# Performance work log

Hardware: AMD Instinct MI355X
Metric: run time of the kernel (lower is better)

The kernel has to match this reference:

```python
import jax, jax.numpy as jnp
import numpy as np

B, L, INP, HID = 32, 1024, 600, 200

def setup_inputs() -> dict:
    key = jax.random.key(0)
    k1, k2, k3, k4 = jax.random.split(key, 4)
    return {
        "s1": jax.random.normal(k1, (B, L, INP), dtype=jnp.float32),
        "s2": jax.random.normal(k2, (B, L, INP), dtype=jnp.float32),
        "mask1": jnp.ones((B, L), dtype=jnp.float32),
        "mask2": jnp.ones((B, L), dtype=jnp.float32),
        "W1": jax.random.normal(k3, (INP, HID), dtype=jnp.float32) * (1.0 / np.sqrt(INP)),
        "b1": jnp.zeros((HID,), dtype=jnp.float32),
        "W2": jax.random.normal(k4, (HID, HID), dtype=jnp.float32) * (1.0 / np.sqrt(HID)),
        "b2": jnp.zeros((HID,), dtype=jnp.float32),
    }

def _mlp(x, W1, b1, W2, b2):
    # Dropout is identity at inference; two Linear+ReLU layers.
    h = jax.nn.relu(x @ W1 + b1)
    return jax.nn.relu(h @ W2 + b2)

def reference(s1, s2, mask1, mask2, W1, b1, W2, b2):
    h1 = _mlp(s1, W1, b1, W2, b2)          # (b, L, hid)
    h2 = _mlp(s2, W1, b1, W2, b2)          # (b, L, hid)
    e = jnp.einsum('bld,bmd->blm', h1, h2) # (b, LA, LB)
    # alpha: mask rows by mask1, softmax over LA (axis=1)
    e_alpha = jax.nn.softmax(e * mask1[:, :, None], axis=1)
    # beta: mask cols by mask2, softmax over LB (axis=2)
    e_beta = jax.nn.softmax(e * mask2[:, None, :], axis=2)
    alphas = jnp.einsum('blm,bld->bmd', e_alpha, s1) * mask2[:, :, None]
    betas = jnp.einsum('blm,bmd->bld', e_beta, s2) * mask1[:, :, None]
    return alphas, betas
```

## Files before the change

kernel.cpp:

```cpp
#include <hip/hip_runtime.h>
#include <hip/hip_bf16.h>
#include <math.h>

namespace {

constexpr int BB  = 32;
constexpr int LL  = 1024;
constexpr int INP = 600;
constexpr int HID = 200;
constexpr int RS  = BB * LL;
constexpr int DPAD = 640;

constexpr int BM = 128, BN = 128, KT = 8;
constexpr int LROW = 40;

typedef __attribute__((ext_vector_type(8))) short short8v;
typedef __attribute__((ext_vector_type(4))) float f32x4;

__device__ __forceinline__ float relu(float x) { return fmaxf(x, 0.f); }

__device__ __forceinline__ unsigned short f2bf(float x) {
  union { float f; unsigned int u; } v; v.f = x;
  unsigned int r = v.u + 0x7FFFu + ((v.u >> 16) & 1u);
  return (unsigned short)(r >> 16);
}
__device__ __forceinline__ float bf2f(unsigned short h) {
  union { unsigned int u; float f; } v; v.u = ((unsigned int)h) << 16;
  return v.f;
}

__device__ __forceinline__ void micro_8x8(const float (&sA)[KT][BM], const float (&sB)[KT][BN],
                                          float (&acc)[8][8], int tx, int ty)
{
#pragma unroll
  for (int kk = 0; kk < KT; ++kk) {
    float4 a0 = *(const float4*)&sA[kk][ty * 8];
    float4 a1 = *(const float4*)&sA[kk][ty * 8 + 4];
    float4 b0 = *(const float4*)&sB[kk][tx * 8];
    float4 b1 = *(const float4*)&sB[kk][tx * 8 + 4];
    float ar[8] = {a0.x, a0.y, a0.z, a0.w, a1.x, a1.y, a1.z, a1.w};
    float br[8] = {b0.x, b0.y, b0.z, b0.w, b1.x, b1.y, b1.z, b1.w};
#pragma unroll
    for (int i = 0; i < 8; ++i)
#pragma unroll
      for (int j = 0; j < 8; ++j)
        acc[i][j] = fmaf(ar[i], br[j], acc[i][j]);
  }
}

__global__ __launch_bounds__(256) void wt_prep(
    const float* __restrict__ W, unsigned short* __restrict__ Whi, unsigned short* __restrict__ Wlo,
    int K, int KP)
{
  const int k = blockIdx.x * 256 + threadIdx.x;
  const int n = blockIdx.y;
  if (k >= KP) return;
  float v = (k < K && n < HID) ? W[(size_t)k * HID + n] : 0.f;
  unsigned short hi = f2bf(v);
  unsigned short lo = f2bf(v - bf2f(hi));
  Whi[(size_t)n * KP + k] = hi;
  Wlo[(size_t)n * KP + k] = lo;
}

__global__ __launch_bounds__(256) void mlp1_gemm_split(
    const float* __restrict__ A0, const float* __restrict__ A1,
    const unsigned short* __restrict__ Bhi, const unsigned short* __restrict__ Blo,
    const float* __restrict__ bias,
    unsigned short* __restrict__ OutHi, unsigned short* __restrict__ OutLo)
{
  __shared__ unsigned short sAhi[128 * LROW], sAlo[128 * LROW];
  __shared__ unsigned short sBhi[128 * LROW], sBlo[128 * LROW];
  const int z = blockIdx.z;
  const float* __restrict__ A = z ? A1 : A0;
  unsigned short* __restrict__ oH = OutHi + (size_t)z * RS * HID;
  unsigned short* __restrict__ oL = OutLo + (size_t)z * RS * HID;
  const int m0 = blockIdx.x * 128, n0 = blockIdx.y * 128;
  const int tid = threadIdx.x, lane = tid & 63;
  const int w = tid >> 6, wr = w >> 1, wc = w & 1;
  const int fr = lane & 15, kg = lane >> 4;

  f32x4 acc[4][4];
#pragma unroll
  for (int mi = 0; mi < 4; ++mi)
#pragma unroll
    for (int ni = 0; ni < 4; ++ni) acc[mi][ni] = (f32x4){0.f, 0.f, 0.f, 0.f};

  for (int k0 = 0; k0 < 608; k0 += 32) {
    __syncthreads();
#pragma unroll
    for (int it = 0; it < 4; ++it) {
      {
        const int t = it * 256 + tid;
        const int r = t >> 3, hc = t & 7;
        const int gk = k0 + hc * 4;
        float4 v = make_float4(0.f, 0.f, 0.f, 0.f);
        if (gk < INP) v = *(const float4*)(A + (size_t)(m0 + r) * INP + gk);
        ushort4 hi, lo;
        hi.x = f2bf(v.x); lo.x = f2bf(v.x - bf2f(hi.x));
        hi.y = f2bf(v.y); lo.y = f2bf(v.y - bf2f(hi.y));
        hi.z = f2bf(v.z); lo.z = f2bf(v.z - bf2f(hi.z));
        hi.w = f2bf(v.w); lo.w = f2bf(v.w - bf2f(hi.w));
        *(ushort4*)&sAhi[r * LROW + hc * 4] = hi;
        *(ushort4*)&sAlo[r * LROW + hc * 4] = lo;
      }
      {
        const int t = it * 256 + tid;
        const bool isLo = t >> 9;
        const int rem = t & 511, r = rem >> 2, c = rem & 3;
        const unsigned short* src = isLo ? Blo : Bhi;
        unsigned short* dst = isLo ? sBlo : sBhi;
        *(int4*)&dst[r * LROW + c * 8] = *(const int4*)(src + (size_t)(n0 + r) * 608 + k0 + c * 8);
      }
    }
    __syncthreads();
    short8v ah[4], al[4], bh[4], bl[4];
#pragma unroll
    for (int mi = 0; mi < 4; ++mi) {
      const int row = wr * 64 + mi * 16 + fr;
      ah[mi] = *(const short8v*)&sAhi[row * LROW + kg * 8];
      al[mi] = *(const short8v*)&sAlo[row * LROW + kg * 8];
    }
#pragma unroll
    for (int ni = 0; ni < 4; ++ni) {
      const int row = wc * 64 + ni * 16 + fr;
      bh[ni] = *(const short8v*)&sBhi[row * LROW + kg * 8];
      bl[ni] = *(const short8v*)&sBlo[row * LROW + kg * 8];
    }
#pragma unroll
    for (int mi = 0; mi < 4; ++mi)
#pragma unroll
      for (int ni = 0; ni < 4; ++ni) {
        acc[mi][ni] = __builtin_amdgcn_mfma_f32_16x16x32_bf16(ah[mi], bh[ni], acc[mi][ni], 0, 0, 0);
        acc[mi][ni] = __builtin_amdgcn_mfma_f32_16x16x32_bf16(ah[mi], bl[ni], acc[mi][ni], 0, 0, 0);
        acc[mi][ni] = __builtin_amdgcn_mfma_f32_16x16x32_bf16(al[mi], bh[ni], acc[mi][ni], 0, 0, 0);
      }
  }
#pragma unroll
  for (int ni = 0; ni < 4; ++ni) {
    const int gn = n0 + wc * 64 + ni * 16 + fr;
    if (gn < HID) {
      const float bs = bias[gn];
#pragma unroll
      for (int mi = 0; mi < 4; ++mi) {
#pragma unroll
        for (int r = 0; r < 4; ++r) {
          const int gm = m0 + wr * 64 + mi * 16 + kg * 4 + r;
          float v = relu(acc[mi][ni][r] + bs);
          unsigned short hi = f2bf(v);
          oH[(size_t)gm * HID + gn] = hi;
          oL[(size_t)gm * HID + gn] = f2bf(v - bf2f(hi));
        }
      }
    }
  }
}

template <bool SPLIT_OUT>
__global__ __launch_bounds__(256) void split_gemm_bf16(
    const unsigned short* __restrict__ Ahi, const unsigned short* __restrict__ Alo,
    int lda, size_t aZ,
    const unsigned short* __restrict__ Bhi, const unsigned short* __restrict__ Blo,
    int ldb, size_t bZ,
    int a_chunks, int b_chunks,
    const float* __restrict__ bias,
    unsigned short* __restrict__ OutHi, unsigned short* __restrict__ OutLo,
    float* __restrict__ OutF, int ldo, size_t oZ)
{
  __shared__ unsigned short sAhi[128 * LROW], sAlo[128 * LROW];
  __shared__ unsigned short sBhi[128 * LROW], sBlo[128 * LROW];
  const int z = blockIdx.z;
  const unsigned short* __restrict__ Ah = Ahi + (size_t)z * aZ;
  const unsigned short* __restrict__ Al = Alo + (size_t)z * aZ;
  const unsigned short* __restrict__ Bh = Bhi + (size_t)z * bZ;
  const unsigned short* __restrict__ Bl = Blo + (size_t)z * bZ;
  const int m0 = blockIdx.x * 128, n0 = blockIdx.y * 128;
  const int tid = threadIdx.x, lane = tid & 63;
  const int w = tid >> 6, wr = w >> 1, wc = w & 1;
  const int fr = lane & 15, kg = lane >> 4;

  f32x4 acc[4][4];
#pragma unroll
  for (int mi = 0; mi < 4; ++mi)
#pragma unroll
    for (int ni = 0; ni < 4; ++ni) acc[mi][ni] = (f32x4){0.f, 0.f, 0.f, 0.f};

  for (int k0 = 0; k0 < 224; k0 += 32) {
    const int kc0 = k0 >> 3;
    __syncthreads();
#pragma unroll
    for (int it = 0; it < 4; ++it) {
      const int t = it * 256 + tid;
      const bool isLo = t >> 9;
      const int rem = t & 511, r = rem >> 2, c = rem & 3;
      const bool av = (kc0 + c) < a_chunks;
      const bool bv = (kc0 + c) < b_chunks;
      int4 va = make_int4(0, 0, 0, 0), vb = make_int4(0, 0, 0, 0);
      if (av) va = *(const int4*)((isLo ? Al : Ah) + (size_t)(m0 + r) * lda + k0 + c * 8);
      if (bv) vb = *(const int4*)((isLo ? Bl : Bh) + (size_t)(n0 + r) * ldb + k0 + c * 8);
      unsigned short* dA = isLo ? sAlo : sAhi;
      unsigned short* dB = isLo ? sBlo : sBhi;
      *(int4*)&dA[r * LROW + c * 8] = va;
      *(int4*)&dB[r * LROW + c * 8] = vb;
    }
    __syncthreads();
    short8v ah[4], al[4], bh[4], bl[4];
#pragma unroll
    for (int mi = 0; mi < 4; ++mi) {
      const int row = wr * 64 + mi * 16 + fr;
      ah[mi] = *(const short8v*)&sAhi[row * LROW + kg * 8];
      al[mi] = *(const short8v*)&sAlo[row * LROW + kg * 8];
    }
#pragma unroll
    for (int ni = 0; ni < 4; ++ni) {
      const int row = wc * 64 + ni * 16 + fr;
      bh[ni] = *(const short8v*)&sBhi[row * LROW + kg * 8];
      bl[ni] = *(const short8v*)&sBlo[row * LROW + kg * 8];
    }
#pragma unroll
    for (int mi = 0; mi < 4; ++mi)
#pragma unroll
      for (int ni = 0; ni < 4; ++ni) {
        acc[mi][ni] = __builtin_amdgcn_mfma_f32_16x16x32_bf16(ah[mi], bh[ni], acc[mi][ni], 0, 0, 0);
        acc[mi][ni] = __builtin_amdgcn_mfma_f32_16x16x32_bf16(ah[mi], bl[ni], acc[mi][ni], 0, 0, 0);
        acc[mi][ni] = __builtin_amdgcn_mfma_f32_16x16x32_bf16(al[mi], bh[ni], acc[mi][ni], 0, 0, 0);
      }
  }
#pragma unroll
  for (int ni = 0; ni < 4; ++ni) {
    const int gn = n0 + wc * 64 + ni * 16 + fr;
    if (!SPLIT_OUT || gn < HID) {
      const float bs = SPLIT_OUT ? bias[gn] : 0.f;
#pragma unroll
      for (int mi = 0; mi < 4; ++mi) {
#pragma unroll
        for (int r = 0; r < 4; ++r) {
          const int gm = m0 + wr * 64 + mi * 16 + kg * 4 + r;
          if (SPLIT_OUT) {
            float v = relu(acc[mi][ni][r] + bs);
            unsigned short hi = f2bf(v);
            OutHi[(size_t)z * oZ + (size_t)gm * ldo + gn] = hi;
            OutLo[(size_t)z * oZ + (size_t)gm * ldo + gn] = f2bf(v - bf2f(hi));
          } else {
            OutF[(size_t)z * oZ + (size_t)gm * ldo + gn] = acc[mi][ni][r];
          }
        }
      }
    }
  }
}

__global__ __launch_bounds__(256) void row_stats_pbeta(
    const float* __restrict__ E, const float* __restrict__ mask2,
    unsigned short* __restrict__ Pb)
{
  const int wid = threadIdx.x >> 6, lane = threadIdx.x & 63;
  const int r = blockIdx.x * 4 + wid;
  const int b = r >> 10;
  const float* __restrict__ row = E + (size_t)r * LL;
  const float* __restrict__ m2 = mask2 + b * LL;
  float v[16];
  float mx = -INFINITY;
#pragma unroll
  for (int i = 0; i < 4; ++i) {
    const int m = lane * 4 + i * 256;
    float4 e4 = *(const float4*)(row + m);
    float4 k4 = *(const float4*)(m2 + m);
    v[i * 4 + 0] = e4.x * k4.x; v[i * 4 + 1] = e4.y * k4.y;
    v[i * 4 + 2] = e4.z * k4.z; v[i * 4 + 3] = e4.w * k4.w;
    mx = fmaxf(mx, fmaxf(fmaxf(v[i * 4], v[i * 4 + 1]), fmaxf(v[i * 4 + 2], v[i * 4 + 3])));
  }
#pragma unroll
  for (int off = 32; off; off >>= 1) mx = fmaxf(mx, __shfl_xor(mx, off));
  float s = 0.f;
#pragma unroll
  for (int i = 0; i < 16; ++i) s += __expf(v[i] - mx);
#pragma unroll
  for (int off = 32; off; off >>= 1) s += __shfl_xor(s, off);
  const float ri = 1.f / s;
#pragma unroll
  for (int i = 0; i < 4; ++i) {
    const int m = lane * 4 + i * 256;
    ushort4 o;
    o.x = f2bf(__expf(v[i * 4 + 0] - mx) * ri);
    o.y = f2bf(__expf(v[i * 4 + 1] - mx) * ri);
    o.z = f2bf(__expf(v[i * 4 + 2] - mx) * ri);
    o.w = f2bf(__expf(v[i * 4 + 3] - mx) * ri);
    *(ushort4*)(Pb + (size_t)r * LL + m) = o;
  }
}

__global__ __launch_bounds__(256) void col_stats_p1(
    const float* __restrict__ E, const float* __restrict__ mask1,
    float* __restrict__ pmax, float* __restrict__ psum)
{
  const int b = blockIdx.z, lc = blockIdx.y;
  const int m = blockIdx.x * 256 + threadIdx.x;
  const float* __restrict__ e = E + (size_t)b * LL * LL;
  const float* __restrict__ m1 = mask1 + b * LL;
  float mx = -INFINITY, s = 0.f;
#pragma unroll 4
  for (int l = lc * 256; l < lc * 256 + 256; ++l) {
    const float v = e[(size_t)l * LL + m] * m1[l];
    if (v > mx) { s = s * __expf(mx - v) + 1.f; mx = v; }
    else        { s += __expf(v - mx); }
  }
  const int idx = (b * 4 + lc) * LL + m;
  pmax[idx] = mx; psum[idx] = s;
}

__global__ __launch_bounds__(256) void col_stats_p2(
    const float* __restrict__ pmax, const float* __restrict__ psum,
    float* __restrict__ cmax, float* __restrict__ cinv)
{
  const int b = blockIdx.y;
  const int m = blockIdx.x * 256 + threadIdx.x;
  float M = -INFINITY;
#pragma unroll
  for (int i = 0; i < 4; ++i) M = fmaxf(M, pmax[(b * 4 + i) * LL + m]);
  float S = 0.f;
#pragma unroll
  for (int i = 0; i < 4; ++i) S += psum[(b * 4 + i) * LL + m] * __expf(pmax[(b * 4 + i) * LL + m] - M);
  cmax[(size_t)b * LL + m] = M;
  cinv[(size_t)b * LL + m] = 1.f / S;
}

__global__ __launch_bounds__(256) void palpha_kernel(
    const float* __restrict__ E, const float* __restrict__ mask1,
    const float* __restrict__ cmax, const float* __restrict__ cinv,
    unsigned short* __restrict__ Pa)
{
  __shared__ float T[64][65];
  const int b = blockIdx.z;
  const int l0 = blockIdx.y * 64, m0 = blockIdx.x * 64;
  const int tid = threadIdx.x;
  const int rr = tid >> 4, c4 = (tid & 15) * 4;
  const float4 cm = *(const float4*)(cmax + b * LL + m0 + c4);
  const float4 ci = *(const float4*)(cinv + b * LL + m0 + c4);
#pragma unroll
  for (int it = 0; it < 4; ++it) {
    const int lloc = rr + it * 16;
    const int l = l0 + lloc;
    const float mk = mask1[b * LL + l];
    const float4 ev = *(const float4*)(E + ((size_t)b * LL + l) * LL + m0 + c4);
    T[c4 + 0][lloc] = __expf(ev.x * mk - cm.x) * ci.x;
    T[c4 + 1][lloc] = __expf(ev.y * mk - cm.y) * ci.y;
    T[c4 + 2][lloc] = __expf(ev.z * mk - cm.z) * ci.z;
    T[c4 + 3][lloc] = __expf(ev.w * mk - cm.w) * ci.w;
  }
  __syncthreads();
#pragma unroll
  for (int it = 0; it < 4; ++it) {
    const int mloc = rr + it * 16;
    ushort4 o;
    o.x = f2bf(T[mloc][c4 + 0]);
    o.y = f2bf(T[mloc][c4 + 1]);
    o.z = f2bf(T[mloc][c4 + 2]);
    o.w = f2bf(T[mloc][c4 + 3]);
    *(ushort4*)(Pa + ((size_t)b * LL + m0 + mloc) * LL + l0 + c4) = o;
  }
}

__global__ __launch_bounds__(256) void s_transpose(
    const float* __restrict__ S, unsigned short* __restrict__ St)
{
  __shared__ float T[64][65];
  const int b = blockIdx.z;
  const int l0 = blockIdx.y * 64, d0 = blockIdx.x * 64;
  const int tid = threadIdx.x;
  const int rr = tid >> 4, c4 = (tid & 15) * 4;
#pragma unroll
  for (int it = 0; it < 4; ++it) {
    const int lloc = rr + it * 16;
    const int l = l0 + lloc;
    float4 v = make_float4(0.f, 0.f, 0.f, 0.f);
    if (d0 + c4 < INP) v = *(const float4*)(S + ((size_t)b * LL + l) * INP + d0 + c4);
    T[c4 + 0][lloc] = v.x; T[c4 + 1][lloc] = v.y;
    T[c4 + 2][lloc] = v.z; T[c4 + 3][lloc] = v.w;
  }
  __syncthreads();
#pragma unroll
  for (int it = 0; it < 4; ++it) {
    const int dloc = rr + it * 16;
    ushort4 o;
    o.x = f2bf(T[dloc][c4 + 0]);
    o.y = f2bf(T[dloc][c4 + 1]);
    o.z = f2bf(T[dloc][c4 + 2]);
    o.w = f2bf(T[dloc][c4 + 3]);
    *(ushort4*)(St + ((size_t)b * DPAD + d0 + dloc) * LL + l0 + c4) = o;
  }
}

__global__ __launch_bounds__(256) void attn_gemm_bf16(
    const unsigned short* __restrict__ Ap, const unsigned short* __restrict__ Bt,
    const float* __restrict__ scale, float* __restrict__ Out)
{
  __shared__ int4 sA4[1024];
  __shared__ int4 sB4[1024];
  __shared__ float s_sc[128];
  const int b  = blockIdx.z;
  const int n0 = blockIdx.x * 128;
  const int m0 = blockIdx.y * 128;
  const int tid = threadIdx.x;
  const int lane = tid & 63;
  const int w = tid >> 6;
  const int wr = w >> 1, wc = w & 1;

  const unsigned short* __restrict__ A  = Ap + (size_t)b * LL * LL;
  const unsigned short* __restrict__ Bp = Bt + (size_t)b * DPAD * LL;

  if (tid < 128) s_sc[tid] = scale[b * LL + m0 + tid];

  f32x4 acc[4][4];
#pragma unroll
  for (int mi = 0; mi < 4; ++mi)
#pragma unroll
    for (int ni = 0; ni < 4; ++ni)
      acc[mi][ni] = (f32x4){0.f, 0.f, 0.f, 0.f};

  const int kc = tid & 7;
  const int rbase = tid >> 3;
  const int fr = lane & 15;
  const int kg = lane >> 4;

  for (int k0 = 0; k0 < LL; k0 += 64) {
    __syncthreads();
#pragma unroll
    for (int it = 0; it < 4; ++it) {
      const int r = rbase + 32 * it;
      sA4[r * 8 + (kc ^ (r & 7))] = *(const int4*)(A  + (size_t)(m0 + r) * LL + k0 + kc * 8);
      sB4[r * 8 + (kc ^ (r & 7))] = *(const int4*)(Bp + (size_t)(n0 + r) * LL + k0 + kc * 8);
    }
    __syncthreads();
#pragma unroll
    for (int kk = 0; kk < 2; ++kk) {
      short8v a[4], bf[4];
#pragma unroll
      for (int mi = 0; mi < 4; ++mi) {
        const int row = wr * 64 + mi * 16 + fr;
        a[mi] = *(const short8v*)&sA4[row * 8 + ((kk * 4 + kg) ^ (row & 7))];
      }
#pragma unroll
      for (int ni = 0; ni < 4; ++ni) {
        const int row = wc * 64 + ni * 16 + fr;
        bf[ni] = *(const short8v*)&sB4[row * 8 + ((kk * 4 + kg) ^ (row & 7))];
      }
#pragma unroll
      for (int mi = 0; mi < 4; ++mi)
#pragma unroll
        for (int ni = 0; ni < 4; ++ni)
          acc[mi][ni] = __builtin_amdgcn_mfma_f32_16x16x32_bf16(a[mi], bf[ni], acc[mi][ni], 0, 0, 0);
    }
  }

#pragma unroll
  for (int mi = 0; mi < 4; ++mi) {
#pragma unroll
    for (int ni = 0; ni < 4; ++ni) {
      const int col = n0 + wc * 64 + ni * 16 + fr;
      if (col < INP) {
#pragma unroll
        for (int r = 0; r < 4; ++r) {
          const int mrow = wr * 64 + mi * 16 + kg * 4 + r;
          Out[((size_t)b * LL + m0 + mrow) * INP + col] = acc[mi][ni][r] * s_sc[mrow];
        }
      }
    }
  }
}

__global__ __launch_bounds__(256) void mlp_gemm(
    const float* __restrict__ A0, const float* __restrict__ A1,
    const float* __restrict__ W,  const float* __restrict__ bias,
    float* __restrict__ Out, int K)
{
  __shared__ __align__(16) float sA[KT][BM];
  __shared__ __align__(16) float sB[KT][BN];
  const int z = blockIdx.z;
  const float* __restrict__ A = z ? A1 : A0;
  float* __restrict__ out = Out + (size_t)z * RS * HID;
  const int m0 = blockIdx.x * BM;
  const int n0 = blockIdx.y * BN;
  const int tid = threadIdx.x;
  const int tx = tid & 15, ty = tid >> 4;
  const int am = tid & 127, akg = (tid >> 7) * 4;
  const int bn = (tid & 31) * 4, bkk = tid >> 5;

  float acc[8][8] = {};
  for (int k0 = 0; k0 < K; k0 += KT) {
    float4 av = *(const float4*)(A + (size_t)(m0 + am) * K + k0 + akg);
    sA[akg + 0][am] = av.x; sA[akg + 1][am] = av.y;
    sA[akg + 2][am] = av.z; sA[akg + 3][am] = av.w;
    const int gn = n0 + bn;
    float4 bv = make_float4(0.f, 0.f, 0.f, 0.f);
    if (gn < HID) bv = *(const float4*)(W + (size_t)(k0 + bkk) * HID + gn);
    *(float4*)&sB[bkk][bn] = bv;
    __syncthreads();
    micro_8x8(sA, sB, acc, tx, ty);
    __syncthreads();
  }
#pragma unroll
  for (int i = 0; i < 8; ++i) {
    const int m = m0 + ty * 8 + i;
#pragma unroll
    for (int j4 = 0; j4 < 8; j4 += 4) {
      const int n = n0 + tx * 8 + j4;
      if (n < HID) {
        float4 v;
        v.x = relu(acc[i][j4 + 0] + bias[n + 0]);
        v.y = relu(acc[i][j4 + 1] + bias[n + 1]);
        v.z = relu(acc[i][j4 + 2] + bias[n + 2]);
        v.w = relu(acc[i][j4 + 3] + bias[n + 3]);
        *(float4*)(out + (size_t)m * HID + n) = v;
      }
    }
  }
}

__global__ __launch_bounds__(256) void e_gemm(
    const float* __restrict__ H1, const float* __restrict__ H2, float* __restrict__ E)
{
  __shared__ __align__(16) float sA[KT][BM];
  __shared__ __align__(16) float sB[KT][BN];
  const int b = blockIdx.z;
  const float* __restrict__ A  = H1 + (size_t)b * LL * HID;
  const float* __restrict__ Bp = H2 + (size_t)b * LL * HID;
  float* __restrict__ e = E + (size_t)b * LL * LL;
  const int l0 = blockIdx.x * BM;
  const int m0 = blockIdx.y * BN;
  const int tid = threadIdx.x;
  const int tx = tid & 15, ty = tid >> 4;
  const int rr = tid & 127, kg = (tid >> 7) * 4;

  float acc[8][8] = {};
  for (int k0 = 0; k0 < HID; k0 += KT) {
    float4 av = *(const float4*)(A + (size_t)(l0 + rr) * HID + k0 + kg);
    sA[kg + 0][rr] = av.x; sA[kg + 1][rr] = av.y;
    sA[kg + 2][rr] = av.z; sA[kg + 3][rr] = av.w;
    float4 bv = *(const float4*)(Bp + (size_t)(m0 + rr) * HID + k0 + kg);
    sB[kg + 0][rr] = bv.x; sB[kg + 1][rr] = bv.y;
    sB[kg + 2][rr] = bv.z; sB[kg + 3][rr] = bv.w;
    __syncthreads();
    micro_8x8(sA, sB, acc, tx, ty);
    __syncthreads();
  }
#pragma unroll
  for (int i = 0; i < 8; ++i) {
    float* erow = e + (size_t)(l0 + ty * 8 + i) * LL + m0 + tx * 8;
    *(float4*)(erow)     = make_float4(acc[i][0], acc[i][1], acc[i][2], acc[i][3]);
    *(float4*)(erow + 4) = make_float4(acc[i][4], acc[i][5], acc[i][6], acc[i][7]);
  }
}

__global__ __launch_bounds__(256) void row_stats(
    const float* __restrict__ E, const float* __restrict__ mask2,
    float* __restrict__ rmax, float* __restrict__ rinv)
{
  const int wid = threadIdx.x >> 6, lane = threadIdx.x & 63;
  const int r = blockIdx.x * 4 + wid;
  const int b = r >> 10;
  const float* __restrict__ row = E + (size_t)r * LL;
  const float* __restrict__ m2 = mask2 + b * LL;
  float v[16];
  float mx = -INFINITY;
#pragma unroll
  for (int i = 0; i < 4; ++i) {
    const int m = lane * 4 + i * 256;
    float4 e4 = *(const float4*)(row + m);
    float4 k4 = *(const float4*)(m2 + m);
    v[i * 4 + 0] = e4.x * k4.x; v[i * 4 + 1] = e4.y * k4.y;
    v[i * 4 + 2] = e4.z * k4.z; v[i * 4 + 3] = e4.w * k4.w;
    mx = fmaxf(mx, fmaxf(fmaxf(v[i * 4], v[i * 4 + 1]), fmaxf(v[i * 4 + 2], v[i * 4 + 3])));
  }
#pragma unroll
  for (int off = 32; off; off >>= 1) mx = fmaxf(mx, __shfl_xor(mx, off));
  float s = 0.f;
#pragma unroll
  for (int i = 0; i < 16; ++i) s += __expf(v[i] - mx);
#pragma unroll
  for (int off = 32; off; off >>= 1) s += __shfl_xor(s, off);
  if (lane == 0) { rmax[r] = mx; rinv[r] = 1.f / s; }
}

__global__ __launch_bounds__(256) void alphas_gemm(
    const float* __restrict__ E, const float* __restrict__ S1,
    const float* __restrict__ mask1, const float* __restrict__ mask2,
    const float* __restrict__ cmax, const float* __restrict__ cinv,
    float* __restrict__ OutA)
{
  __shared__ __align__(16) float sA[KT][BM];
  __shared__ __align__(16) float sB[KT][BN];
  __shared__ __align__(16) float s_cm[BM], s_ci[BM], s_m2[BM];
  const int b = blockIdx.z;
  const float* __restrict__ e  = E  + (size_t)b * LL * LL;
  const float* __restrict__ s1 = S1 + (size_t)b * LL * INP;
  const int m0 = blockIdx.x * BM;
  const int d0 = blockIdx.y * BN;
  const int tid = threadIdx.x;
  const int tx = tid & 15, ty = tid >> 4;
  if (tid < BM) {
    s_cm[tid] = cmax[b * LL + m0 + tid];
    s_ci[tid] = cinv[b * LL + m0 + tid];
    s_m2[tid] = mask2[b * LL + m0 + tid];
  }
  __syncthreads();
  const int cc = (tid & 31) * 4, kk_ = tid >> 5;

  float acc[8][8] = {};
  for (int k0 = 0; k0 < LL; k0 += KT) {
    const int l = k0 + kk_;
    const float mk = mask1[b * LL + l];
    float4 ev = *(const float4*)(e + (size_t)l * LL + m0 + cc);
    float4 av;
    av.x = __expf(ev.x * mk - s_cm[cc + 0]) * s_ci[cc + 0];
    av.y = __expf(ev.y * mk - s_cm[cc + 1]) * s_ci[cc + 1];
    av.z = __expf(ev.z * mk - s_cm[cc + 2]) * s_ci[cc + 2];
    av.w = __expf(ev.w * mk - s_cm[cc + 3]) * s_ci[cc + 3];
    *(float4*)&sA[kk_][cc] = av;
    const int gd = d0 + cc;
    float4 bv = make_float4(0.f, 0.f, 0.f, 0.f);
    if (gd < INP) bv = *(const float4*)(s1 + (size_t)l * INP + gd);
    *(float4*)&sB[kk_][cc] = bv;
    __syncthreads();
    micro_8x8(sA, sB, acc, tx, ty);
    __syncthreads();
  }
#pragma unroll
  for (int i = 0; i < 8; ++i) {
    const int m = m0 + ty * 8 + i;
    const float mm = s_m2[ty * 8 + i];
    float* orow = OutA + ((size_t)b * LL + m) * INP;
#pragma unroll
    for (int j4 = 0; j4 < 8; j4 += 4) {
      const int d = d0 + tx * 8 + j4;
      if (d < INP) {
        *(float4*)(orow + d) = make_float4(acc[i][j4] * mm, acc[i][j4 + 1] * mm,
                                           acc[i][j4 + 2] * mm, acc[i][j4 + 3] * mm);
      }
    }
  }
}

__global__ __launch_bounds__(256) void betas_gemm(
    const float* __restrict__ E, const float* __restrict__ S2,
    const float* __restrict__ mask1, const float* __restrict__ mask2,
    const float* __restrict__ rmax, const float* __restrict__ rinv,
    float* __restrict__ OutB)
{
  __shared__ __align__(16) float sA[KT][BM];
  __shared__ __align__(16) float sB[KT][BN];
  __shared__ __align__(16) float s_rm[BM], s_ri[BM], s_m1[BM];
  const int b = blockIdx.z;
  const float* __restrict__ e  = E  + (size_t)b * LL * LL;
  const float* __restrict__ s2 = S2 + (size_t)b * LL * INP;
  const int l0 = blockIdx.x * BM;
  const int d0 = blockIdx.y * BN;
  const int tid = threadIdx.x;
  const int tx = tid & 15, ty = tid >> 4;
  if (tid < BM) {
    s_rm[tid] = rmax[b * LL + l0 + tid];
    s_ri[tid] = rinv[b * LL + l0 + tid];
    s_m1[tid] = mask1[b * LL + l0 + tid];
  }
  __syncthreads();
  const int al = tid & 127, akg = (tid >> 7) * 4;
  const int cc = (tid & 31) * 4, kk_ = tid >> 5;

  float acc[8][8] = {};
  for (int k0 = 0; k0 < LL; k0 += KT) {
    float4 ev = *(const float4*)(e + (size_t)(l0 + al) * LL + k0 + akg);
    float4 mk = *(const float4*)(mask2 + b * LL + k0 + akg);
    const float rm = s_rm[al], ri = s_ri[al];
    sA[akg + 0][al] = __expf(ev.x * mk.x - rm) * ri;
    sA[akg + 1][al] = __expf(ev.y * mk.y - rm) * ri;
    sA[akg + 2][al] = __expf(ev.z * mk.z - rm) * ri;
    sA[akg + 3][al] = __expf(ev.w * mk.w - rm) * ri;
    const int gd = d0 + cc;
    float4 bv = make_float4(0.f, 0.f, 0.f, 0.f);
    if (gd < INP) bv = *(const float4*)(s2 + (size_t)(k0 + kk_) * INP + gd);
    *(float4*)&sB[kk_][cc] = bv;
    __syncthreads();
    micro_8x8(sA, sB, acc, tx, ty);
    __syncthreads();
  }
#pragma unroll
  for (int i = 0; i < 8; ++i) {
    const int l = l0 + ty * 8 + i;
    const float mm = s_m1[ty * 8 + i];
    float* orow = OutB + ((size_t)b * LL + l) * INP;
#pragma unroll
    for (int j4 = 0; j4 < 8; j4 += 4) {
      const int d = d0 + tx * 8 + j4;
      if (d < INP) {
        *(float4*)(orow + d) = make_float4(acc[i][j4] * mm, acc[i][j4 + 1] * mm,
                                           acc[i][j4 + 2] * mm, acc[i][j4 + 3] * mm);
      }
    }
  }
}

}

extern "C" void kernel_launch(void* const* d_in, const int* in_sizes, int n_in,
                              void* d_out, int out_size, void* d_ws, size_t ws_size,
                              hipStream_t stream)
{
  const float* s1    = (const float*)d_in[0];
  const float* s2    = (const float*)d_in[1];
  const float* mask1 = (const float*)d_in[2];
  const float* mask2 = (const float*)d_in[3];
  const float* W1    = (const float*)d_in[4];
  const float* b1    = (const float*)d_in[5];
  const float* W2    = (const float*)d_in[6];
  const float* b2    = (const float*)d_in[7];

  char* ws = (char*)d_ws;
  float* outA = (float*)d_out;
  float* outB = outA + (size_t)BB * LL * INP;

  const size_t off_hmid = 0;
  const size_t off_h    = 52428800;
  const size_t off_E    = 104857600;
  const size_t off_Pb   = 239075328;
  const size_t TOTAL    = 306184192;

  if (ws_size >= TOTAL) {
    unsigned short* hmid_hi = (unsigned short*)(ws + off_hmid);
    unsigned short* hmid_lo = hmid_hi + (size_t)2 * RS * HID;
    unsigned short* h_hi    = (unsigned short*)(ws + off_h);
    unsigned short* h_lo    = h_hi + (size_t)2 * RS * HID;
    float* E = (float*)(ws + off_E);
    unsigned short* Wt1hi = (unsigned short*)(ws + off_E);
    unsigned short* Wt1lo = Wt1hi + (size_t)256 * 608;
    unsigned short* Wt2hi = Wt1lo + (size_t)256 * 608;
    unsigned short* Wt2lo = Wt2hi + (size_t)256 * 224;
    unsigned short* Pb = (unsigned short*)(ws + off_Pb);
    unsigned short* Pa = (unsigned short*)(ws + 0);
    float* stats = (float*)(ws + 67108864);
    float* cmax = stats;
    float* cinv = cmax + RS;
    float* pmax = cinv + RS;
    float* psum = pmax + (size_t)BB * 4 * LL;
    unsigned short* s1t = (unsigned short*)(ws + off_E);
    unsigned short* s2t = s1t + (size_t)BB * DPAD * LL;

    wt_prep<<<dim3(3, 256), 256, 0, stream>>>(W1, Wt1hi, Wt1lo, INP, 608);
    wt_prep<<<dim3(1, 256), 256, 0, stream>>>(W2, Wt2hi, Wt2lo, HID, 224);
    mlp1_gemm_split<<<dim3(RS / 128, 2, 2), 256, 0, stream>>>(
        s1, s2, Wt1hi, Wt1lo, b1, hmid_hi, hmid_lo);
    split_gemm_bf16<true><<<dim3(RS / 128, 2, 2), 256, 0, stream>>>(
        hmid_hi, hmid_lo, HID, (size_t)RS * HID,
        Wt2hi, Wt2lo, 224, 0,
        25, 28, b2, h_hi, h_lo, nullptr, HID, (size_t)RS * HID);
    split_gemm_bf16<false><<<dim3(8, 8, BB), 256, 0, stream>>>(
        h_hi, h_lo, HID, (size_t)LL * HID,
        h_hi + (size_t)RS * HID, h_lo + (size_t)RS * HID, HID, (size_t)LL * HID,
        25, 25, nullptr, nullptr, nullptr, E, LL, (size_t)LL * LL);
    row_stats_pbeta<<<dim3(RS / 4), 256, 0, stream>>>(E, mask2, Pb);
    col_stats_p1<<<dim3(4, 4, BB), 256, 0, stream>>>(E, mask1, pmax, psum);
    col_stats_p2<<<dim3(4, BB), 256, 0, stream>>>(pmax, psum, cmax, cinv);
    palpha_kernel<<<dim3(16, 16, BB), 256, 0, stream>>>(E, mask1, cmax, cinv, Pa);
    s_transpose<<<dim3(10, 16, BB), 256, 0, stream>>>(s1, s1t);
    s_transpose<<<dim3(10, 16, BB), 256, 0, stream>>>(s2, s2t);
    attn_gemm_bf16<<<dim3(5, 8, BB), 256, 0, stream>>>(Pb, s2t, mask1, outB);
    attn_gemm_bf16<<<dim3(5, 8, BB), 256, 0, stream>>>(Pa, s1t, mask2, outA);
  } else {
    float* h    = (float*)ws;
    float* hmid = h + (size_t)2 * RS * HID;
    float* E    = hmid;
    float* stats = hmid + (size_t)BB * LL * LL;
    float* rmax = stats;
    float* rinv = rmax + RS;
    float* cmax = rinv + RS;
    float* cinv = cmax + RS;
    float* pmax = cinv + RS;
    float* psum = pmax + (size_t)BB * 4 * LL;

    mlp_gemm<<<dim3(RS / BM, 2, 2), 256, 0, stream>>>(s1, s2, W1, b1, hmid, INP);
    mlp_gemm<<<dim3(RS / BM, 2, 2), 256, 0, stream>>>(hmid, hmid + (size_t)RS * HID, W2, b2, h, HID);
    e_gemm<<<dim3(LL / BM, LL / BN, BB), 256, 0, stream>>>(h, h + (size_t)RS * HID, E);
    row_stats<<<dim3(RS / 4), 256, 0, stream>>>(E, mask2, rmax, rinv);
    col_stats_p1<<<dim3(4, 4, BB), 256, 0, stream>>>(E, mask1, pmax, psum);
    col_stats_p2<<<dim3(4, BB), 256, 0, stream>>>(pmax, psum, cmax, cinv);
    alphas_gemm<<<dim3(LL / BM, (INP + BN - 1) / BN, BB), 256, 0, stream>>>(
        E, s1, mask1, mask2, cmax, cinv, outA);
    betas_gemm<<<dim3(LL / BM, (INP + BN - 1) / BN, BB), 256, 0, stream>>>(
        E, s2, mask1, mask2, rmax, rinv, outB);
  }

  (void)in_sizes; (void)n_in; (void)out_size;
}
```

Measured before the change: 946.2 us.

## Unify split-bf16 GEMMs with on-the-fly fp32 splitting and async LDS loads

Replaces the separate MLP and split GEMM kernels with one templated kernel. Each tile of fp32 operands is loaded and split into bf16 hi/lo pairs inside the kernel, so intermediates are stored as fp32 rather than pre-split hi/lo arrays. It also moves to 64-wide K steps with an XOR-swizzled shared layout instead of padded rows. Weight tiles and the attention GEMM operands are loaded with global_load_lds direct-to-LDS transfers, which removes register staging. The cost is redundant conversion arithmetic per tile, extra zero-padded K work (W1 padded to 640, W2 to 256), and the LDS layout now depends on the builtin's per-wave placement.

New measurement: 926.4 us. 1.02x faster.

```diff
diff --git a/kernel.cpp b/kernel.cpp
--- a/kernel.cpp
+++ b/kernel.cpp
@@ -1,5 +1,4 @@
 #include <hip/hip_runtime.h>
-#include <hip/hip_bf16.h>
 #include <math.h>
 
 namespace {
@@ -12,9 +11,9 @@
 constexpr int DPAD = 640;
 
 constexpr int BM = 128, BN = 128, KT = 8;
-constexpr int LROW = 40;
 
 typedef __attribute__((ext_vector_type(8))) short short8v;
+typedef __attribute__((ext_vector_type(8))) unsigned short ushort8v;
 typedef __attribute__((ext_vector_type(4))) float f32x4;
 
 __device__ __forceinline__ float relu(float x) { return fmaxf(x, 0.f); }
@@ -29,23 +28,9 @@
   return v.f;
 }
 
-__device__ __forceinline__ void micro_8x8(const float (&sA)[KT][BM], const float (&sB)[KT][BN],
-                                          float (&acc)[8][8], int tx, int ty)
-{
-#pragma unroll
-  for (int kk = 0; kk < KT; ++kk) {
-    float4 a0 = *(const float4*)&sA[kk][ty * 8];
-    float4 a1 = *(const float4*)&sA[kk][ty * 8 + 4];
-    float4 b0 = *(const float4*)&sB[kk][tx * 8];
-    float4 b1 = *(const float4*)&sB[kk][tx * 8 + 4];
-    float ar[8] = {a0.x, a0.y, a0.z, a0.w, a1.x, a1.y, a1.z, a1.w};
-    float br[8] = {b0.x, b0.y, b0.z, b0.w, b1.x, b1.y, b1.z, b1.w};
-#pragma unroll
-    for (int i = 0; i < 8; ++i)
-#pragma unroll
-      for (int j = 0; j < 8; ++j)
-        acc[i][j] = fmaf(ar[i], br[j], acc[i][j]);
-  }
+__device__ __forceinline__ void gload16(const void* g, void* l) {
+  __builtin_amdgcn_global_load_lds((const __attribute__((address_space(1))) void*)g,
+                                   (__attribute__((address_space(3))) void*)l, 16, 0, 0);
 }
 
 __global__ __launch_bounds__(256) void wt_prep(
@@ -62,22 +47,26 @@
   Wlo[(size_t)n * KP + k] = lo;
 }
 
-__global__ __launch_bounds__(256) void mlp1_gemm_split(
-    const float* __restrict__ A0, const float* __restrict__ A1,
+template <bool MLP>
+__global__ __launch_bounds__(256) void splitmm(
+    const float* __restrict__ A0, const float* __restrict__ A1, long aZ, int lda, int ka,
+    const float* __restrict__ Bf, long bZ,
     const unsigned short* __restrict__ Bhi, const unsigned short* __restrict__ Blo,
+    int ldb, int kb, int ksteps,
     const float* __restrict__ bias,
-    unsigned short* __restrict__ OutHi, unsigned short* __restrict__ OutLo)
-{
-  __shared__ unsigned short sAhi[128 * LROW], sAlo[128 * LROW];
-  __shared__ unsigned short sBhi[128 * LROW], sBlo[128 * LROW];
+    float* __restrict__ Out, int ldo, long oZ)
+{
+  __shared__ int4 sA[2048];
+  __shared__ int4 sB[2048];
   const int z = blockIdx.z;
-  const float* __restrict__ A = z ? A1 : A0;
-  unsigned short* __restrict__ oH = OutHi + (size_t)z * RS * HID;
-  unsigned short* __restrict__ oL = OutLo + (size_t)z * RS * HID;
   const int m0 = blockIdx.x * 128, n0 = blockIdx.y * 128;
-  const int tid = threadIdx.x, lane = tid & 63;
-  const int w = tid >> 6, wr = w >> 1, wc = w & 1;
-  const int fr = lane & 15, kg = lane >> 4;
+  const int tid = threadIdx.x, lane = tid & 63, w = tid >> 6;
+  const int wr = w >> 1, wc = w & 1, fr = lane & 15, kg = lane >> 4;
+
+  const float* __restrict__ A = MLP ? (z ? A1 : A0) : (A0 + (size_t)z * aZ);
+  const float* __restrict__ Bp = MLP ? (const float*)nullptr : (Bf + (size_t)z * bZ);
+
+  const int ar = tid >> 1, aseg = tid & 1;
 
   f32x4 acc[4][4];
 #pragma unroll
@@ -85,164 +74,107 @@
 #pragma unroll
     for (int ni = 0; ni < 4; ++ni) acc[mi][ni] = (f32x4){0.f, 0.f, 0.f, 0.f};
 
-  for (int k0 = 0; k0 < 608; k0 += 32) {
-    __syncthreads();
-#pragma unroll
-    for (int it = 0; it < 4; ++it) {
-      {
-        const int t = it * 256 + tid;
-        const int r = t >> 3, hc = t & 7;
-        const int gk = k0 + hc * 4;
-        float4 v = make_float4(0.f, 0.f, 0.f, 0.f);
-        if (gk < INP) v = *(const float4*)(A + (size_t)(m0 + r) * INP + gk);
-        ushort4 hi, lo;
-        hi.x = f2bf(v.x); lo.x = f2bf(v.x - bf2f(hi.x));
-        hi.y = f2bf(v.y); lo.y = f2bf(v.y - bf2f(hi.y));
-        hi.z = f2bf(v.z); lo.z = f2bf(v.z - bf2f(hi.z));
-        hi.w = f2bf(v.w); lo.w = f2bf(v.w - bf2f(hi.w));
-        *(ushort4*)&sAhi[r * LROW + hc * 4] = hi;
-        *(ushort4*)&sAlo[r * LROW + hc * 4] = lo;
-      }
-      {
-        const int t = it * 256 + tid;
-        const bool isLo = t >> 9;
-        const int rem = t & 511, r = rem >> 2, c = rem & 3;
-        const unsigned short* src = isLo ? Blo : Bhi;
-        unsigned short* dst = isLo ? sBlo : sBhi;
-        *(int4*)&dst[r * LROW + c * 8] = *(const int4*)(src + (size_t)(n0 + r) * 608 + k0 + c * 8);
-      }
-    }
-    __syncthreads();
-    short8v ah[4], al[4], bh[4], bl[4];
-#pragma unroll
-    for (int mi = 0; mi < 4; ++mi) {
-      const int row = wr * 64 + mi * 16 + fr;
-      ah[mi] = *(const short8v*)&sAhi[row * LROW + kg * 8];
-      al[mi] = *(const short8v*)&sAlo[row * LROW + kg * 8];
-    }
-#pragma unroll
-    for (int ni = 0; ni < 4; ++ni) {
-      const int row = wc * 64 + ni * 16 + fr;
-      bh[ni] = *(const short8v*)&sBhi[row * LROW + kg * 8];
-      bl[ni] = *(const short8v*)&sBlo[row * LROW + kg * 8];
-    }
-#pragma unroll
-    for (int mi = 0; mi < 4; ++mi)
+  for (int ks = 0; ks < ksteps; ++ks) {
+    const int k0 = ks * 64;
+    __syncthreads();
+#pragma unroll
+    for (int u = 0; u < 4; ++u) {
+      const int c = aseg * 4 + u;
+      const int gk = k0 + c * 8;
+      float4 v0 = make_float4(0.f, 0.f, 0.f, 0.f), v1 = v0;
+      if (gk < ka) {
+        const float* p = A + (size_t)(m0 + ar) * lda + gk;
+        v0 = *(const float4*)p;
+        v1 = *(const float4*)(p + 4);
+      }
+      ushort8v hv, lv;
+      hv[0] = f2bf(v0.x); lv[0] = f2bf(v0.x - bf2f(hv[0]));
+      hv[1] = f2bf(v0.y); lv[1] = f2bf(v0.y - bf2f(hv[1]));
+      hv[2] = f2bf(v0.z); lv[2] = f2bf(v0.z - bf2f(hv[2]));
+      hv[3] = f2bf(v0.w); lv[3] = f2bf(v0.w - bf2f(hv[3]));
+      hv[4] = f2bf(v1.x); lv[4] = f2bf(v1.x - bf2f(hv[4]));
+      hv[5] = f2bf(v1.y); lv[5] = f2bf(v1.y - bf2f(hv[5]));
+      hv[6] = f2bf(v1.z); lv[6] = f2bf(v1.z - bf2f(hv[6]));
+      hv[7] = f2bf(v1.w); lv[7] = f2bf(v1.w - bf2f(hv[7]));
+      const int slot = ar * 8 + (c ^ (ar & 7));
+      *(ushort8v*)&sA[slot] = hv;
+      *(ushort8v*)&sA[1024 + slot] = lv;
+    }
+    if (MLP) {
+#pragma unroll
+      for (int i = 0; i < 8; ++i) {
+        const int s = w * 512 + i * 64 + lane;
+        const int tens = s >> 10, rem = s & 1023, r = rem >> 3, kc = rem & 7;
+        const int gc = kc ^ (r & 7);
+        const unsigned short* src = (tens ? Blo : Bhi) + (size_t)(n0 + r) * ldb + k0 + gc * 8;
+        gload16(src, (char*)sB + ((size_t)(w * 512 + i * 64)) * 16);
+      }
+    } else {
+#pragma unroll
+      for (int u = 0; u < 4; ++u) {
+        const int c = aseg * 4 + u;
+        const int gk = k0 + c * 8;
+        float4 v0 = make_float4(0.f, 0.f, 0.f, 0.f), v1 = v0;
+        if (gk < kb) {
+          const float* p = Bp + (size_t)(n0 + ar) * ldb + gk;
+          v0 = *(const float4*)p;
+          v1 = *(const float4*)(p + 4);
+        }
+        ushort8v hv, lv;
+        hv[0] = f2bf(v0.x); lv[0] = f2bf(v0.x - bf2f(hv[0]));
+        hv[1] = f2bf(v0.y); lv[1] = f2bf(v0.y - bf2f(hv[1]));
+        hv[2] = f2bf(v0.z); lv[2] = f2bf(v0.z - bf2f(hv[2]));
+        hv[3] = f2bf(v0.w); lv[3] = f2bf(v0.w - bf2f(hv[3]));
+        hv[4] = f2bf(v1.x); lv[4] = f2bf(v1.x - bf2f(hv[4]));
+        hv[5] = f2bf(v1.y); lv[5] = f2bf(v1.y - bf2f(hv[5]));
+        hv[6] = f2bf(v1.z); lv[6] = f2bf(v1.z - bf2f(hv[6]));
+        hv[7] = f2bf(v1.w); lv[7] = f2bf(v1.w - bf2f(hv[7]));
+        const int slot = ar * 8 + (c ^ (ar & 7));
+        *(ushort8v*)&sB[slot] = hv;
+        *(ushort8v*)&sB[1024 + slot] = lv;
+      }
+    }
+    __syncthreads();
+#pragma unroll
+    for (int kk = 0; kk < 2; ++kk) {
+      short8v ah[4], al[4], bh[4], bl[4];
+#pragma unroll
+      for (int mi = 0; mi < 4; ++mi) {
+        const int row = wr * 64 + mi * 16 + fr;
+        const int idx = row * 8 + ((kk * 4 + kg) ^ (row & 7));
+        ah[mi] = *(const short8v*)&sA[idx];
+        al[mi] = *(const short8v*)&sA[1024 + idx];
+      }
 #pragma unroll
       for (int ni = 0; ni < 4; ++ni) {
-        acc[mi][ni] = __builtin_amdgcn_mfma_f32_16x16x32_bf16(ah[mi], bh[ni], acc[mi][ni], 0, 0, 0);
-        acc[mi][ni] = __builtin_amdgcn_mfma_f32_16x16x32_bf16(ah[mi], bl[ni], acc[mi][ni], 0, 0, 0);
-        acc[mi][ni] = __builtin_amdgcn_mfma_f32_16x16x32_bf16(al[mi], bh[ni], acc[mi][ni], 0, 0, 0);
-      }
+        const int row = wc * 64 + ni * 16 + fr;
+        const int idx = row * 8 + ((kk * 4 + kg) ^ (row & 7));
+        bh[ni] = *(const short8v*)&sB[idx];
+        bl[ni] = *(const short8v*)&sB[1024 + idx];
+      }
+#pragma unroll
+      for (int mi = 0; mi < 4; ++mi)
+#pragma unroll
+        for (int ni = 0; ni < 4; ++ni) {
+          acc[mi][ni] = __builtin_amdgcn_mfma_f32_16x16x32_bf16(ah[mi], bh[ni], acc[mi][ni], 0, 0, 0);
+          acc[mi][ni] = __builtin_amdgcn_mfma_f32_16x16x32_bf16(ah[mi], bl[ni], acc[mi][ni], 0, 0, 0);
+          acc[mi][ni] = __builtin_amdgcn_mfma_f32_16x16x32_bf16(al[mi], bh[ni], acc[mi][ni], 0, 0, 0);
+        }
+    }
   }
 #pragma unroll
   for (int ni = 0; ni < 4; ++ni) {
     const int gn = n0 + wc * 64 + ni * 16 + fr;
-    if (gn < HID) {
-      const float bs = bias[gn];
+    if (!MLP || gn < HID) {
+      const float bs = MLP ? bias[gn] : 0.f;
 #pragma unroll
       for (int mi = 0; mi < 4; ++mi) {
 #pragma unroll
         for (int r = 0; r < 4; ++r) {
           const int gm = m0 + wr * 64 + mi * 16 + kg * 4 + r;
-          float v = relu(acc[mi][ni][r] + bs);
-          unsigned short hi = f2bf(v);
-          oH[(size_t)gm * HID + gn] = hi;
-          oL[(size_t)gm * HID + gn] = f2bf(v - bf2f(hi));
-        }
-      }
-    }
-  }
-}
-
-template <bool SPLIT_OUT>
-__global__ __launch_bounds__(256) void split_gemm_bf16(
-    const unsigned short* __restrict__ Ahi, const unsigned short* __restrict__ Alo,
-    int lda, size_t aZ,
-    const unsigned short* __restrict__ Bhi, const unsigned short* __restrict__ Blo,
-    int ldb, size_t bZ,
-    int a_chunks, int b_chunks,
-    const float* __restrict__ bias,
-    unsigned short* __restrict__ OutHi, unsigned short* __restrict__ OutLo,
-    float* __restrict__ OutF, int ldo, size_t oZ)
-{
-  __shared__ unsigned short sAhi[128 * LROW], sAlo[128 * LROW];
-  __shared__ unsigned short sBhi[128 * LROW], sBlo[128 * LROW];
-  const int z = blockIdx.z;
-  const unsigned short* __restrict__ Ah = Ahi + (size_t)z * aZ;
-  const unsigned short* __restrict__ Al = Alo + (size_t)z * aZ;
-  const unsigned short* __restrict__ Bh = Bhi + (size_t)z * bZ;
-  const unsigned short* __restrict__ Bl = Blo + (size_t)z * bZ;
-  const int m0 = blockIdx.x * 128, n0 = blockIdx.y * 128;
-  const int tid = threadIdx.x, lane = tid & 63;
-  const int w = tid >> 6, wr = w >> 1, wc = w & 1;
-  const int fr = lane & 15, kg = lane >> 4;
-
-  f32x4 acc[4][4];
-#pragma unroll
-  for (int mi = 0; mi < 4; ++mi)
-#pragma unroll
-    for (int ni = 0; ni < 4; ++ni) acc[mi][ni] = (f32x4){0.f, 0.f, 0.f, 0.f};
-
-  for (int k0 = 0; k0 < 224; k0 += 32) {
-    const int kc0 = k0 >> 3;
-    __syncthreads();
-#pragma unroll
-    for (int it = 0; it < 4; ++it) {
-      const int t = it * 256 + tid;
-      const bool isLo = t >> 9;
-      const int rem = t & 511, r = rem >> 2, c = rem & 3;
-      const bool av = (kc0 + c) < a_chunks;
-      const bool bv = (kc0 + c) < b_chunks;
-      int4 va = make_int4(0, 0, 0, 0), vb = make_int4(0, 0, 0, 0);
-      if (av) va = *(const int4*)((isLo ? Al : Ah) + (size_t)(m0 + r) * lda + k0 + c * 8);
-      if (bv) vb = *(const int4*)((isLo ? Bl : Bh) + (size_t)(n0 + r) * ldb + k0 + c * 8);
-      unsigned short* dA = isLo ? sAlo : sAhi;
-      unsigned short* dB = isLo ? sBlo : sBhi;
-      *(int4*)&dA[r * LROW + c * 8] = va;
-      *(int4*)&dB[r * LROW + c * 8] = vb;
-    }
-    __syncthreads();
-    short8v ah[4], al[4], bh[4], bl[4];
-#pragma unroll
-    for (int mi = 0; mi < 4; ++mi) {
-      const int row = wr * 64 + mi * 16 + fr;
-      ah[mi] = *(const short8v*)&sAhi[row * LROW + kg * 8];
-      al[mi] = *(const short8v*)&sAlo[row * LROW + kg * 8];
-    }
-#pragma unroll
-    for (int ni = 0; ni < 4; ++ni) {
-      const int row = wc * 64 + ni * 16 + fr;
-      bh[ni] = *(const short8v*)&sBhi[row * LROW + kg * 8];
-      bl[ni] = *(const short8v*)&sBlo[row * LROW + kg * 8];
-    }
-#pragma unroll
-    for (int mi = 0; mi < 4; ++mi)
-#pragma unroll
-      for (int ni = 0; ni < 4; ++ni) {
-        acc[mi][ni] = __builtin_amdgcn_mfma_f32_16x16x32_bf16(ah[mi], bh[ni], acc[mi][ni], 0, 0, 0);
-        acc[mi][ni] = __builtin_amdgcn_mfma_f32_16x16x32_bf16(ah[mi], bl[ni], acc[mi][ni], 0, 0, 0);
-        acc[mi][ni] = __builtin_amdgcn_mfma_f32_16x16x32_bf16(al[mi], bh[ni], acc[mi][ni], 0, 0, 0);
-      }
-  }
-#pragma unroll
-  for (int ni = 0; ni < 4; ++ni) {
-    const int gn = n0 + wc * 64 + ni * 16 + fr;
-    if (!SPLIT_OUT || gn < HID) {
-      const float bs = SPLIT_OUT ? bias[gn] : 0.f;
-#pragma unroll
-      for (int mi = 0; mi < 4; ++mi) {
-#pragma unroll
-        for (int r = 0; r < 4; ++r) {
-          const int gm = m0 + wr * 64 + mi * 16 + kg * 4 + r;
-          if (SPLIT_OUT) {
-            float v = relu(acc[mi][ni][r] + bs);
-            unsigned short hi = f2bf(v);
-            OutHi[(size_t)z * oZ + (size_t)gm * ldo + gn] = hi;
-            OutLo[(size_t)z * oZ + (size_t)gm * ldo + gn] = f2bf(v - bf2f(hi));
-          } else {
-            OutF[(size_t)z * oZ + (size_t)gm * ldo + gn] = acc[mi][ni][r];
-          }
+          float v = acc[mi][ni][r] + bs;
+          if (MLP) v = relu(v);
+          Out[(size_t)z * oZ + (size_t)gm * ldo + gn] = v;
         }
       }
     }
@@ -394,8 +326,7 @@
     const unsigned short* __restrict__ Ap, const unsigned short* __restrict__ Bt,
     const float* __restrict__ scale, float* __restrict__ Out)
 {
-  __shared__ int4 sA4[1024];
-  __shared__ int4 sB4[1024];
+  __shared__ int4 sAB[2048];
   __shared__ float s_sc[128];
   const int b  = blockIdx.z;
   const int n0 = blockIdx.x * 128;
@@ -404,6 +335,7 @@
   const int lane = tid & 63;
   const int w = tid >> 6;
   const int wr = w >> 1, wc = w & 1;
+  const int fr = lane & 15, kg = lane >> 4;
 
   const unsigned short* __restrict__ A  = Ap + (size_t)b * LL * LL;
   const unsigned short* __restrict__ Bp = Bt + (size_t)b * DPAD * LL;
@@ -417,18 +349,16 @@
     for (int ni = 0; ni < 4; ++ni)
       acc[mi][ni] = (f32x4){0.f, 0.f, 0.f, 0.f};
 
-  const int kc = tid & 7;
-  const int rbase = tid >> 3;
-  const int fr = lane & 15;
-  const int kg = lane >> 4;
-
   for (int k0 = 0; k0 < LL; k0 += 64) {
     __syncthreads();
 #pragma unroll
-    for (int it = 0; it < 4; ++it) {
-      const int r = rbase + 32 * it;
-      sA4[r * 8 + (kc ^ (r & 7))] = *(const int4*)(A  + (size_t)(m0 + r) * LL + k0 + kc * 8);
-      sB4[r * 8 + (kc ^ (r & 7))] = *(const int4*)(Bp + (size_t)(n0 + r) * LL + k0 + kc * 8);
+    for (int i = 0; i < 8; ++i) {
+      const int s = w * 512 + i * 64 + lane;
+      const int tens = s >> 10, rem = s & 1023, r = rem >> 3, kc = rem & 7;
+      const int gc = kc ^ (r & 7);
+      const unsigned short* src = tens ? (Bp + (size_t)(n0 + r) * LL + k0 + gc * 8)
+                                       : (A  + (size_t)(m0 + r) * LL + k0 + gc * 8);
+      gload16(src, (char*)sAB + ((size_t)(w * 512 + i * 64)) * 16);
     }
     __syncthreads();
 #pragma unroll
@@ -437,12 +367,12 @@
 #pragma unroll
       for (int mi = 0; mi < 4; ++mi) {
         const int row = wr * 64 + mi * 16 + fr;
-        a[mi] = *(const short8v*)&sA4[row * 8 + ((kk * 4 + kg) ^ (row & 7))];
+        a[mi] = *(const short8v*)&sAB[row * 8 + ((kk * 4 + kg) ^ (row & 7))];
       }
 #pragma unroll
       for (int ni = 0; ni < 4; ++ni) {
         const int row = wc * 64 + ni * 16 + fr;
-        bf[ni] = *(const short8v*)&sB4[row * 8 + ((kk * 4 + kg) ^ (row & 7))];
+        bf[ni] = *(const short8v*)&sAB[1024 + row * 8 + ((kk * 4 + kg) ^ (row & 7))];
       }
 #pragma unroll
       for (int mi = 0; mi < 4; ++mi)
@@ -465,6 +395,25 @@
         }
       }
     }
+  }
+}
+
+__device__ __forceinline__ void micro_8x8(const float (&sA)[KT][BM], const float (&sB)[KT][BN],
+                                          float (&acc)[8][8], int tx, int ty)
+{
+#pragma unroll
+  for (int kk = 0; kk < KT; ++kk) {
+    float4 a0 = *(const float4*)&sA[kk][ty * 8];
+    float4 a1 = *(const float4*)&sA[kk][ty * 8 + 4];
+    float4 b0 = *(const float4*)&sB[kk][tx * 8];
+    float4 b1 = *(const float4*)&sB[kk][tx * 8 + 4];
+    float ar[8] = {a0.x, a0.y, a0.z, a0.w, a1.x, a1.y, a1.z, a1.w};
+    float br[8] = {b0.x, b0.y, b0.z, b0.w, b1.x, b1.y, b1.z, b1.w};
+#pragma unroll
+    for (int i = 0; i < 8; ++i)
+#pragma unroll
+      for (int j = 0; j < 8; ++j)
+        acc[i][j] = fmaf(ar[i], br[j], acc[i][j]);
   }
 }
 
@@ -717,22 +666,19 @@
   float* outA = (float*)d_out;
   float* outB = outA + (size_t)BB * LL * INP;
 
-  const size_t off_hmid = 0;
-  const size_t off_h    = 52428800;
-  const size_t off_E    = 104857600;
-  const size_t off_Pb   = 239075328;
-  const size_t TOTAL    = 306184192;
+  const size_t off_h  = 52428800;
+  const size_t off_E  = 104857600;
+  const size_t off_Pb = 239075328;
+  const size_t TOTAL  = 306184192;
 
   if (ws_size >= TOTAL) {
-    unsigned short* hmid_hi = (unsigned short*)(ws + off_hmid);
-    unsigned short* hmid_lo = hmid_hi + (size_t)2 * RS * HID;
-    unsigned short* h_hi    = (unsigned short*)(ws + off_h);
-    unsigned short* h_lo    = h_hi + (size_t)2 * RS * HID;
-    float* E = (float*)(ws + off_E);
+    float* hmid = (float*)(ws + 0);
+    float* h    = (float*)(ws + off_h);
+    float* E    = (float*)(ws + off_E);
     unsigned short* Wt1hi = (unsigned short*)(ws + off_E);
-    unsigned short* Wt1lo = Wt1hi + (size_t)256 * 608;
-    unsigned short* Wt2hi = Wt1lo + (size_t)256 * 608;
-    unsigned short* Wt2lo = Wt2hi + (size_t)256 * 224;
+    unsigned short* Wt1lo = Wt1hi + (size_t)256 * 640;
+    unsigned short* Wt2hi = Wt1lo + (size_t)256 * 640;
+    unsigned short* Wt2lo = Wt2hi + (size_t)256 * 256;
     unsigned short* Pb = (unsigned short*)(ws + off_Pb);
     unsigned short* Pa = (unsigned short*)(ws + 0);
     float* stats = (float*)(ws + 67108864);
@@ -743,18 +689,18 @@
     unsigned short* s1t = (unsigned short*)(ws + off_E);
     unsigned short* s2t = s1t + (size_t)BB * DPAD * LL;
 
-    wt_prep<<<dim3(3, 256), 256, 0, stream>>>(W1, Wt1hi, Wt1lo, INP, 608);
-    wt_prep<<<dim3(1, 256), 256, 0, stream>>>(W2, Wt2hi, Wt2lo, HID, 224);
-    mlp1_gemm_split<<<dim3(RS / 128, 2, 2), 256, 0, stream>>>(
-        s1, s2, Wt1hi, Wt1lo, b1, hmid_hi, hmid_lo);
-    split_gemm_bf16<true><<<dim3(RS / 128, 2, 2), 256, 0, stream>>>(
-        hmid_hi, hmid_lo, HID, (size_t)RS * HID,
-        Wt2hi, Wt2lo, 224, 0,
-        25, 28, b2, h_hi, h_lo, nullptr, HID, (size_t)RS * HID);
-    split_gemm_bf16<false><<<dim3(8, 8, BB), 256, 0, stream>>>(
-        h_hi, h_lo, HID, (size_t)LL * HID,
-        h_hi + (size_t)RS * HID, h_lo + (size_t)RS * HID, HID, (size_t)LL * HID,
-        25, 25, nullptr, nullptr, nullptr, E, LL, (size_t)LL * LL);
+    wt_prep<<<dim3(3, 256), 256, 0, stream>>>(W1, Wt1hi, Wt1lo, INP, 640);
+    wt_prep<<<dim3(1, 256), 256, 0, stream>>>(W2, Wt2hi, Wt2lo, HID, 256);
+    splitmm<true><<<dim3(RS / 128, 2, 2), 256, 0, stream>>>(
+        s1, s2, 0, INP, INP, nullptr, 0, Wt1hi, Wt1lo, 640, 0, 10,
+        b1, hmid, HID, (long)RS * HID);
+    splitmm<true><<<dim3(RS / 128, 2, 2), 256, 0, stream>>>(
+        hmid, hmid + (size_t)RS * HID, 0, HID, HID, nullptr, 0, Wt2hi, Wt2lo, 256, 0, 4,
+        b2, h, HID, (long)RS * HID);
+    splitmm<false><<<dim3(8, 8, BB), 256, 0, stream>>>(
+        h, nullptr, (long)LL * HID, HID, HID,
+        h + (size_t)RS * HID, (long)LL * HID, nullptr, nullptr, HID, HID, 4,
+        nullptr, E, LL, (long)LL * LL);
     row_stats_pbeta<<<dim3(RS / 4), 256, 0, stream>>>(E, mask2, Pb);
     col_stats_p1<<<dim3(4, 4, BB), 256, 0, stream>>>(E, mask1, pmax, psum);
     col_stats_p2<<<dim3(4, BB), 256, 0, stream>>>(pmax, psum, cmax, cinv);
```
